# Optimization experiments

Measured on AMD Instinct MI355X. Metric: run time of the kernel, lower is better.

Reference implementation:

```python
import jax, jax.numpy as jnp
import numpy as np

B, S, D, H, E = 1, 2048, 1024, 16, 65536
HD = D // H
LN_EPS = 1e-5


def setup_inputs() -> dict:
    key = jax.random.key(0)
    ks = jax.random.split(key, 18)
    s = 0.02
    inp = {
        'x': jax.random.normal(ks[0], (B, S, D), jnp.float32),
        'node_types': jax.random.uniform(ks[1], (B, S, 2), jnp.float32),
        'stoichiometry': jax.random.normal(ks[2], (E,), jnp.float32),
        'Wq': s * jax.random.normal(ks[3], (D, D), jnp.float32),
        'bq': jnp.zeros((D,), jnp.float32),
        'Wk': s * jax.random.normal(ks[4], (D, D), jnp.float32),
        'bk': jnp.zeros((D,), jnp.float32),
        'Wv': s * jax.random.normal(ks[5], (D, D), jnp.float32),
        'bv': jnp.zeros((D,), jnp.float32),
        'Wo': s * jax.random.normal(ks[6], (D, D), jnp.float32),
        'bo': jnp.zeros((D,), jnp.float32),
        'Wn1': s * jax.random.normal(ks[7], (D // 2, D + 2), jnp.float32),
        'bn1': jnp.zeros((D // 2,), jnp.float32),
        'Wn2': s * jax.random.normal(ks[8], (H, D // 2), jnp.float32),
        'bn2': jnp.zeros((H,), jnp.float32),
        'ln_g': jnp.ones((D,), jnp.float32),
        'ln_b': jnp.zeros((D,), jnp.float32),
        'edge_index': jax.random.randint(ks[9], (2, E), 0, S, jnp.int64),
    }
    return inp


def _layer_norm(y, g, b):
    m = jnp.mean(y, axis=-1, keepdims=True)
    v = jnp.mean(jnp.square(y - m), axis=-1, keepdims=True)
    return (y - m) * jax.lax.rsqrt(v + LN_EPS) * g + b


def reference(x, node_types, stoichiometry, Wq, bq, Wk, bk, Wv, bv, Wo, bo,
              Wn1, bn1, Wn2, bn2, ln_g, ln_b, edge_index):
    b, s, d = x.shape
    h, hd = H, d // H
    # QKV projections -> [b, h, s, hd]
    Q = (x @ Wq.T + bq).reshape(b, s, h, hd).transpose(0, 2, 1, 3)
    K = (x @ Wk.T + bk).reshape(b, s, h, hd).transpose(0, 2, 1, 3)
    V = (x @ Wv.T + bv).reshape(b, s, h, hd).transpose(0, 2, 1, 3)
    scores = jnp.einsum('bhqd,bhkd->bhqk', Q, K) / np.sqrt(hd)  # [b,h,s,s]
    # node-type attention MLP -> per-node, per-head weights [b,s,h]
    nt_in = jnp.concatenate([x, node_types], axis=-1)
    ntw = jax.nn.softmax(jax.nn.relu(nt_in @ Wn1.T + bn1) @ Wn2.T + bn2, axis=-1)
    # applied as per-head, per-key multiplicative mask [b,h,1,s]
    scores = scores * ntw.transpose(0, 2, 1)[:, :, None, :]
    # dense stoichiometric mask via edge scatter [s,s]
    stoich_mask = jnp.zeros((s, s), x.dtype).at[edge_index[0], edge_index[1]].set(stoichiometry)
    scores = scores * stoich_mask[None, None]
    attn = jax.nn.softmax(scores, axis=-1)  # dropout = identity (eval)
    out = jnp.einsum('bhqk,bhkd->bhqd', attn, V).transpose(0, 2, 1, 3).reshape(b, s, d)
    out = out @ Wo.T + bo
    y = _layer_norm(x + out, ln_g, ln_b)
    return (y, attn)
```

## Files before the change

### kernel.cpp

```cpp
#include <hip/hip_runtime.h>
#include <hip/hip_bf16.h>

#define S 2048
#define D 1024
#define NH 16
#define HD 64
#define NE 65536
#define DH 512
#define SLOTS 128

typedef __attribute__((ext_vector_type(8))) short short8;
typedef __attribute__((ext_vector_type(4))) float f32x4;

#define MFMA16(a, b, c) __builtin_amdgcn_mfma_f32_16x16x32_bf16(a, b, c, 0, 0, 0)

__device__ __forceinline__ unsigned short f2bf(float f) {
    __hip_bfloat16 h = __float2bfloat16(f);
    return *reinterpret_cast<unsigned short*>(&h);
}
__device__ __forceinline__ float bf2f(unsigned short u) {
    unsigned int x = ((unsigned int)u) << 16;
    return *reinterpret_cast<float*>(&x);
}

__device__ __forceinline__ void gload16(const unsigned short* g, unsigned short* l) {
    __builtin_amdgcn_global_load_lds(
        (const __attribute__((address_space(1))) unsigned int*)g,
        (__attribute__((address_space(3))) unsigned int*)l, 16, 0, 0);
}

__global__ __launch_bounds__(256) void k_prep(const float* __restrict__ x,
                                              const float* __restrict__ Wq,
                                              const float* __restrict__ Wk,
                                              const float* __restrict__ Wv,
                                              const float* __restrict__ Wn1,
                                              const float* __restrict__ Wo,
                                              const float* __restrict__ bq,
                                              const float* __restrict__ bk,
                                              const float* __restrict__ bv,
                                              const float* __restrict__ bn1,
                                              unsigned short* __restrict__ xb,
                                              unsigned short* __restrict__ wb,
                                              float* __restrict__ biasAll,
                                              int* __restrict__ rowcnt) {
    int row = blockIdx.x, z = blockIdx.y, t = threadIdx.x;
    if (z == 5) {
        if (row < 14) {
            int g = row * 256 + t;
            float v = (g < 1024) ? bq[g]
                    : (g < 2048) ? bk[g - 1024]
                    : (g < 3072) ? bv[g - 2048] : bn1[g - 3072];
            biasAll[g] = v;
        } else if (row >= 16 && row < 24) {
            rowcnt[(row - 16) * 256 + t] = 0;
        }
        return;
    }
    if (z >= 6) {
        int s = (z - 6) * 1024 + row;
        const float* r = x + (long)s * 1024;
        unsigned short* o = xb + (long)s * 1024;
#pragma unroll
        for (int j = 0; j < 4; j++) o[t * 4 + j] = f2bf(r[t * 4 + j]);
        return;
    }
    if (z == 3 && row >= DH) return;
    const float* src;
    long stride = 1024;
    if (z == 0) src = Wq;
    else if (z == 1) src = Wk;
    else if (z == 2) src = Wv;
    else if (z == 3) { src = Wn1; stride = 1026; }
    else src = Wo;
    const float* r = src + (long)row * stride;
    unsigned short* o = wb + (long)z * 1048576 + (long)row * 1024;
#pragma unroll
    for (int j = 0; j < 4; j++) o[t * 4 + j] = f2bf(r[t * 4 + j]);
}

__global__ __launch_bounds__(256) void k_scatter_csr(const int* __restrict__ ei,
                                                     const float* __restrict__ st,
                                                     int* __restrict__ rowcnt,
                                                     int* __restrict__ cpack,
                                                     float* __restrict__ cval) {
    int e = blockIdx.x * 256 + threadIdx.x;
    int r = ei[e], c = ei[NE + e];
    int i = atomicAdd(&rowcnt[r], 1);
    if (i < SLOTS) {
        cpack[r * SLOTS + i] = ((e + 1) << 11) | c;
        cval[r * SLOTS + i] = st[e];
    }
}

__global__ __launch_bounds__(256) void k_gemm_fused(const unsigned short* __restrict__ A,
                                                    const unsigned short* __restrict__ Bw,
                                                    const float* __restrict__ biasAll,
                                                    unsigned short* __restrict__ qout,
                                                    unsigned short* __restrict__ kout,
                                                    unsigned short* __restrict__ vout,
                                                    float* __restrict__ hidden) {
    __shared__ unsigned short Als[128 * 64];
    __shared__ unsigned short Bls[128 * 64];
    const int tid = threadIdx.x, w = tid >> 6, lane = tid & 63;
    const int l15 = lane & 15, lhi = lane >> 4;
    const int wr = w >> 1, wc = w & 1;
    const int m0 = blockIdx.x * 128, n0 = blockIdx.y * 128;
    f32x4 acc[4][4] = {};
    for (int kt = 0; kt < 16; kt++) {
        __syncthreads();
#pragma unroll
        for (int i = 0; i < 4; i++) {
            int reg = i * 4 + w;
            int idx = reg * 64 + lane;
            int row = idx >> 3, c8 = (idx & 7) * 8;
            gload16(A + (long)(m0 + row) * 1024 + kt * 64 + c8, Als + reg * 512);
            gload16(Bw + (long)(n0 + row) * 1024 + kt * 64 + c8, Bls + reg * 512);
        }
        asm volatile("s_waitcnt vmcnt(0)");
        __syncthreads();
#pragma unroll
        for (int kk = 0; kk < 2; kk++) {
            short8 a[4], b[4];
#pragma unroll
            for (int mi = 0; mi < 4; mi++)
                a[mi] = *reinterpret_cast<const short8*>(Als + (wr * 64 + mi * 16 + l15) * 64 + kk * 32 + lhi * 8);
#pragma unroll
            for (int ni = 0; ni < 4; ni++)
                b[ni] = *reinterpret_cast<const short8*>(Bls + (wc * 64 + ni * 16 + l15) * 64 + kk * 32 + lhi * 8);
#pragma unroll
            for (int mi = 0; mi < 4; mi++)
#pragma unroll
                for (int ni = 0; ni < 4; ni++)
                    acc[mi][ni] = MFMA16(a[mi], b[ni], acc[mi][ni]);
        }
    }
#pragma unroll
    for (int ni = 0; ni < 4; ni++) {
        int n = n0 + wc * 64 + ni * 16 + l15;
        float bb = biasAll[n];
#pragma unroll
        for (int mi = 0; mi < 4; mi++) {
#pragma unroll
            for (int r = 0; r < 4; r++) {
                int m = m0 + wr * 64 + mi * 16 + lhi * 4 + r;
                float v = acc[mi][ni][r] + bb;
                if (n < 3072) {
                    int z = n >> 10, c = n & 1023;
                    int hh = c >> 6, hd = c & 63;
                    unsigned short* dst = (z == 0) ? qout : ((z == 1) ? kout : vout);
                    dst[(long)hh * S * HD + (long)m * HD + hd] = f2bf(v);
                } else {
                    hidden[(long)m * DH + (n - 3072)] = v;
                }
            }
        }
    }
}

__global__ __launch_bounds__(256) void k_gemm_out(const unsigned short* __restrict__ A,
                                                  const unsigned short* __restrict__ Bw,
                                                  const float* __restrict__ bo,
                                                  float* __restrict__ proj) {
    __shared__ unsigned short Als[128 * 64];
    __shared__ unsigned short Bls[64 * 64];
    const int tid = threadIdx.x, w = tid >> 6, lane = tid & 63;
    const int l15 = lane & 15, lhi = lane >> 4;
    const int wr = w >> 1, wc = w & 1;
    const int m0 = blockIdx.x * 128, n0 = blockIdx.y * 64;
    f32x4 acc[4][2] = {};
    for (int kt = 0; kt < 16; kt++) {
        __syncthreads();
#pragma unroll
        for (int i = 0; i < 4; i++) {
            int reg = i * 4 + w;
            int idx = reg * 64 + lane;
            int row = idx >> 3, c8 = (idx & 7) * 8;
            gload16(A + (long)(m0 + row) * 1024 + kt * 64 + c8, Als + reg * 512);
        }
#pragma unroll
        for (int i = 0; i < 2; i++) {
            int reg = i * 4 + w;
            int idx = reg * 64 + lane;
            int row = idx >> 3, c8 = (idx & 7) * 8;
            gload16(Bw + (long)(n0 + row) * 1024 + kt * 64 + c8, Bls + reg * 512);
        }
        asm volatile("s_waitcnt vmcnt(0)");
        __syncthreads();
#pragma unroll
        for (int kk = 0; kk < 2; kk++) {
            short8 a[4], b[2];
#pragma unroll
            for (int mi = 0; mi < 4; mi++)
                a[mi] = *reinterpret_cast<const short8*>(Als + (wr * 64 + mi * 16 + l15) * 64 + kk * 32 + lhi * 8);
#pragma unroll
            for (int ni = 0; ni < 2; ni++)
                b[ni] = *reinterpret_cast<const short8*>(Bls + (wc * 32 + ni * 16 + l15) * 64 + kk * 32 + lhi * 8);
#pragma unroll
            for (int mi = 0; mi < 4; mi++)
#pragma unroll
                for (int ni = 0; ni < 2; ni++)
                    acc[mi][ni] = MFMA16(a[mi], b[ni], acc[mi][ni]);
        }
    }
#pragma unroll
    for (int ni = 0; ni < 2; ni++) {
        int n = n0 + wc * 32 + ni * 16 + l15;
        float bb = bo[n];
#pragma unroll
        for (int mi = 0; mi < 4; mi++) {
#pragma unroll
            for (int r = 0; r < 4; r++) {
                int m = m0 + wr * 64 + mi * 16 + lhi * 4 + r;
                proj[(long)m * 1024 + n] = acc[mi][ni][r] + bb;
            }
        }
    }
}

__global__ __launch_bounds__(256) void k_ntw(const float* __restrict__ hidden,
                                             const float* __restrict__ Wn1,
                                             const float* __restrict__ nt,
                                             const float* __restrict__ Wn2,
                                             const float* __restrict__ bn2,
                                             const unsigned short* __restrict__ vb,
                                             float* __restrict__ ntwT,
                                             float* __restrict__ vsump) {
    int tid = threadIdx.x;
    if (blockIdx.x >= 2048) {
        int idx = blockIdx.x - 2048;
        int h = idx >> 3, j = idx & 7;
        int w = tid >> 6, lane = tid & 63;
        __shared__ float p[4][64];
        float acc = 0.f;
        int r0 = j * 256 + w * 64;
        for (int k = 0; k < 64; k++)
            acc += bf2f(vb[((long)h * S + r0 + k) * HD + lane]);
        p[w][lane] = acc;
        __syncthreads();
        if (tid < 64) vsump[(h * 8 + j) * 64 + tid] = p[0][tid] + p[1][tid] + p[2][tid] + p[3][tid];
        return;
    }
    int s = blockIdx.x;
    __shared__ float rh[DH];
    __shared__ float part[16][17];
    float nt0 = nt[s * 2 + 0], nt1 = nt[s * 2 + 1];
    for (int j = tid; j < DH; j += 256) {
        float v = hidden[(long)s * DH + j] + nt0 * Wn1[(long)j * 1026 + 1024]
                + nt1 * Wn1[(long)j * 1026 + 1025];
        rh[j] = fmaxf(v, 0.f);
    }
    __syncthreads();
    {
        int hh = tid & 15, ch = tid >> 4;
        float p2 = 0.f;
#pragma unroll
        for (int j = 0; j < 32; j++) p2 += rh[ch * 32 + j] * Wn2[hh * DH + ch * 32 + j];
        part[ch][hh] = p2;
    }
    __syncthreads();
    if (tid < 16) {
        float l = bn2[tid];
#pragma unroll
        for (int c = 0; c < 16; c++) l += part[c][tid];
        float mx = l;
#pragma unroll
        for (int m = 1; m < 16; m <<= 1) mx = fmaxf(mx, __shfl_xor(mx, m));
        float e = __expf(l - mx);
        float sum = e;
#pragma unroll
        for (int m = 1; m < 16; m <<= 1) sum += __shfl_xor(sum, m);
        ntwT[tid * S + s] = e / sum;
    }
}

__global__ __launch_bounds__(256, 4) void k_sparsefill(const unsigned short* __restrict__ qb,
                                                       const unsigned short* __restrict__ kb,
                                                       const unsigned short* __restrict__ vb,
                                                       const float* __restrict__ ntwT,
                                                       const int* __restrict__ rowcnt,
                                                       const int* __restrict__ cpack,
                                                       const float* __restrict__ cval,
                                                       const float* __restrict__ vsump,
                                                       float* __restrict__ attn_out,
                                                       unsigned short* __restrict__ pv_out) {
    __shared__ int c_lds[4][SLOTS];
    __shared__ float pd_lds[4][SLOTS];
    __shared__ unsigned char alive_lds[4][SLOTS];
    const int tid = threadIdx.x, w = tid >> 6, lane = tid & 63;
    int b = (int)blockIdx.x;
    b = (b & 7) * 1024 + (b >> 3);
    const int r = b * 4 + w;
    const int h = r >> 11, q = r & 2047;
    const int i_loc = lane & 15, dpart = lane >> 4;
    const int nnz_raw = rowcnt[q];
    const int nnz = nnz_raw < SLOTS ? nnz_raw : SLOTS;
    const int chunks = (nnz + 15) >> 4;

    for (int i = lane; i < nnz; i += 64) c_lds[w][i] = cpack[q * SLOTS + i];
    asm volatile("" ::: "memory");

    int myCnt = 0;
    for (int i = lane; i < nnz; i += 64) {
        int pk = c_lds[w][i];
        bool alive = true;
        for (int j = 0; j < nnz; j++) {
            int pj = c_lds[w][j];
            if ((((pj ^ pk) & 2047) == 0) && pj > pk) alive = false;
        }
        alive_lds[w][i] = alive ? 1 : 0;
        myCnt += alive ? 1 : 0;
    }
#pragma unroll
    for (int off = 1; off < 64; off <<= 1) myCnt += __shfl_xor(myCnt, off);
    const int nnz_alive = myCnt;
    asm volatile("" ::: "memory");

    float qf[16];
    {
        const unsigned short* qp = qb + ((long)h * S + q) * HD + dpart * 16;
        short8 q0 = *reinterpret_cast<const short8*>(qp);
        short8 q1 = *reinterpret_cast<const short8*>(qp + 8);
#pragma unroll
        for (int j = 0; j < 8; j++) {
            qf[j] = bf2f((unsigned short)q0[j]);
            qf[8 + j] = bf2f((unsigned short)q1[j]);
        }
    }

    float s_reg[8], e_reg[8];
    int c_reg[8];
    int vmask = 0;
#pragma unroll
    for (int c8 = 0; c8 < 8; c8++) {
        s_reg[c8] = -3.0e38f;
        c_reg[c8] = 0;
        if (c8 < chunks) {
            int i = c8 * 16 + i_loc;
            bool inr = i < nnz;
            int ig = inr ? i : 0;
            bool valid = inr && alive_lds[w][ig];
            int c = c_lds[w][ig] & 2047;
            float vv = cval[q * SLOTS + ig];
            const unsigned short* kp = kb + ((long)h * S + c) * HD + dpart * 16;
            short8 k0 = *reinterpret_cast<const short8*>(kp);
            short8 k1 = *reinterpret_cast<const short8*>(kp + 8);
            float dot = 0.f;
#pragma unroll
            for (int j = 0; j < 8; j++) {
                dot += qf[j] * bf2f((unsigned short)k0[j]);
                dot += qf[8 + j] * bf2f((unsigned short)k1[j]);
            }
            dot += __shfl_xor(dot, 16);
            dot += __shfl_xor(dot, 32);
            if (valid) {
                s_reg[c8] = dot * 0.125f * ntwT[(long)h * S + c] * vv;
                c_reg[c8] = c;
                vmask |= 1 << c8;
            }
        }
    }

    float m = s_reg[0];
#pragma unroll
    for (int c8 = 1; c8 < 8; c8++) m = fmaxf(m, s_reg[c8]);
    m = fmaxf(m, __shfl_xor(m, 1));
    m = fmaxf(m, __shfl_xor(m, 2));
    m = fmaxf(m, __shfl_xor(m, 4));
    m = fmaxf(m, __shfl_xor(m, 8));
    const float gm = fmaxf(m, 0.f);

    float zs = 0.f;
#pragma unroll
    for (int c8 = 0; c8 < 8; c8++) {
        e_reg[c8] = __expf(s_reg[c8] - gm);
        zs += e_reg[c8];
    }
    zs += __shfl_xor(zs, 1);
    zs += __shfl_xor(zs, 2);
    zs += __shfl_xor(zs, 4);
    zs += __shfl_xor(zs, 8);
    const float e0 = __expf(-gm);
    const float Z = zs + (float)(S - nnz_alive) * e0;
    const float inv = 1.0f / Z;
    const float p0 = e0 * inv;

    if (dpart == 0) {
#pragma unroll
        for (int c8 = 0; c8 < 8; c8++) {
            int i = c8 * 16 + i_loc;
            if (c8 < chunks && i < nnz)
                pd_lds[w][i] = ((vmask >> c8) & 1) ? e_reg[c8] * inv - p0 : 0.f;
        }
    }
    asm volatile("" ::: "memory");

    float* arow = attn_out + (long)r * S;
    float4* a4 = reinterpret_cast<float4*>(arow) + lane;
    const float4 f4 = {p0, p0, p0, p0};
#pragma unroll
    for (int u = 0; u < 8; u++) a4[u * 64] = f4;
    __threadfence_block();
    if (dpart == 0) {
#pragma unroll
        for (int c8 = 0; c8 < 8; c8++)
            if ((vmask >> c8) & 1) arow[c_reg[c8]] = e_reg[c8] * inv;
    }

    float vacc = 0.f;
    for (int i = 0; i < nnz; i++) {
        int c = c_lds[w][i] & 2047;
        float pd = pd_lds[w][i];
        vacc += pd * bf2f(vb[((long)h * S + c) * HD + lane]);
    }
    float vs = 0.f;
#pragma unroll
    for (int j = 0; j < 8; j++) vs += vsump[(h * 8 + j) * 64 + lane];
    vacc += p0 * vs;
    pv_out[(long)q * D + h * HD + lane] = f2bf(vacc);
}

__global__ __launch_bounds__(256) void k_ln(const float* __restrict__ x,
                                            const float* __restrict__ proj,
                                            const float* __restrict__ g,
                                            const float* __restrict__ bta,
                                            float* __restrict__ y) {
    int s = blockIdx.x, tid = threadIdx.x;
    int w = tid >> 6, lane = tid & 63;
    __shared__ float red[8];
    float4 xv = reinterpret_cast<const float4*>(x + (long)s * 1024)[tid];
    float4 pv = reinterpret_cast<const float4*>(proj + (long)s * 1024)[tid];
    float t0 = xv.x + pv.x, t1 = xv.y + pv.y, t2 = xv.z + pv.z, t3 = xv.w + pv.w;
    float lsum = t0 + t1 + t2 + t3;
#pragma unroll
    for (int m = 32; m >= 1; m >>= 1) lsum += __shfl_xor(lsum, m);
    if (lane == 0) red[w] = lsum;
    __syncthreads();
    float mean = (red[0] + red[1] + red[2] + red[3]) * (1.0f / 1024.f);
    float d0 = t0 - mean, d1 = t1 - mean, d2 = t2 - mean, d3 = t3 - mean;
    float lvar = d0 * d0 + d1 * d1 + d2 * d2 + d3 * d3;
#pragma unroll
    for (int m = 32; m >= 1; m >>= 1) lvar += __shfl_xor(lvar, m);
    if (lane == 0) red[4 + w] = lvar;
    __syncthreads();
    float var = (red[4] + red[5] + red[6] + red[7]) * (1.0f / 1024.f);
    float rstd = rsqrtf(var + 1e-5f);
    float4 gv = reinterpret_cast<const float4*>(g)[tid];
    float4 bv = reinterpret_cast<const float4*>(bta)[tid];
    float4 out;
    out.x = d0 * rstd * gv.x + bv.x;
    out.y = d1 * rstd * gv.y + bv.y;
    out.z = d2 * rstd * gv.z + bv.z;
    out.w = d3 * rstd * gv.w + bv.w;
    reinterpret_cast<float4*>(y + (long)s * 1024)[tid] = out;
}

extern "C" void kernel_launch(void* const* d_in, const int* in_sizes, int n_in,
                              void* d_out, int out_size, void* d_ws, size_t ws_size,
                              hipStream_t stream) {
    const float* x = (const float*)d_in[0];
    const float* node_types = (const float*)d_in[1];
    const float* stoich = (const float*)d_in[2];
    const float* Wq = (const float*)d_in[3];
    const float* bq = (const float*)d_in[4];
    const float* Wk = (const float*)d_in[5];
    const float* bk = (const float*)d_in[6];
    const float* Wv = (const float*)d_in[7];
    const float* bv = (const float*)d_in[8];
    const float* Wo = (const float*)d_in[9];
    const float* bo = (const float*)d_in[10];
    const float* Wn1 = (const float*)d_in[11];
    const float* bn1 = (const float*)d_in[12];
    const float* Wn2 = (const float*)d_in[13];
    const float* bn2 = (const float*)d_in[14];
    const float* ln_g = (const float*)d_in[15];
    const float* ln_b = (const float*)d_in[16];
    const int* ei = (const int*)d_in[17];

    char* ws = (char*)d_ws;
    unsigned short* x_bf = (unsigned short*)(ws);
    unsigned short* q_bf = (unsigned short*)(ws + (4l << 20));
    unsigned short* k_bf = (unsigned short*)(ws + (8l << 20));
    unsigned short* v_bf = (unsigned short*)(ws + (12l << 20));
    unsigned short* w_bf = (unsigned short*)(ws + (16l << 20));
    float* hidden = (float*)(ws + (26l << 20));
    float* ntwT = (float*)(ws + (30l << 20));
    int* rowcnt = (int*)(ws + (30l << 20) + (192l << 10));
    float* vsump = (float*)(ws + (30l << 20) + (384l << 10));
    float* biasAll = (float*)(ws + (30l << 20) + (448l << 10));
    int* cpack = (int*)(ws + (31l << 20));
    float* cval = (float*)(ws + (32l << 20));
    unsigned short* pvb = (unsigned short*)(ws + (49l << 20));
    float* proj = (float*)(ws + (53l << 20));

    float* y_out = (float*)d_out;
    float* attn_out = (float*)d_out + (long)S * D;

    k_prep<<<dim3(1024, 8), 256, 0, stream>>>(x, Wq, Wk, Wv, Wn1, Wo,
                                              bq, bk, bv, bn1, x_bf, w_bf,
                                              biasAll, rowcnt);
    k_scatter_csr<<<256, 256, 0, stream>>>(ei, stoich, rowcnt, cpack, cval);
    k_gemm_fused<<<dim3(16, 28), 256, 0, stream>>>(x_bf, w_bf, biasAll,
                                                   q_bf, k_bf, v_bf, hidden);
    k_ntw<<<2176, 256, 0, stream>>>(hidden, Wn1, node_types, Wn2, bn2, v_bf,
                                    ntwT, vsump);
    k_sparsefill<<<8192, 256, 0, stream>>>(q_bf, k_bf, v_bf, ntwT, rowcnt,
                                           cpack, cval, vsump, attn_out, pvb);
    k_gemm_out<<<dim3(16, 16), 256, 0, stream>>>(pvb, w_bf + 4l * 1048576, bo, proj);
    k_ln<<<2048, 256, 0, stream>>>(x, proj, ln_g, ln_b, y_out);
}
```

Before: 161.3 us.

## Fuse edge scatter and V column sums into the QKV GEMM kernel

```diff
diff --git a/kernel.cpp b/kernel.cpp
--- a/kernel.cpp
+++ b/kernel.cpp
@@ -42,7 +42,8 @@
                                               unsigned short* __restrict__ xb,
                                               unsigned short* __restrict__ wb,
                                               float* __restrict__ biasAll,
-                                              int* __restrict__ rowcnt) {
+                                              int* __restrict__ rowcnt,
+                                              float* __restrict__ vsumf) {
     int row = blockIdx.x, z = blockIdx.y, t = threadIdx.x;
     if (z == 5) {
         if (row < 14) {
@@ -53,6 +54,8 @@
             biasAll[g] = v;
         } else if (row >= 16 && row < 24) {
             rowcnt[(row - 16) * 256 + t] = 0;
+        } else if (row >= 24 && row < 28) {
+            vsumf[(row - 24) * 256 + t] = 0.f;
         }
         return;
     }
@@ -78,27 +81,33 @@
     for (int j = 0; j < 4; j++) o[t * 4 + j] = f2bf(r[t * 4 + j]);
 }
 
-__global__ __launch_bounds__(256) void k_scatter_csr(const int* __restrict__ ei,
-                                                     const float* __restrict__ st,
-                                                     int* __restrict__ rowcnt,
-                                                     int* __restrict__ cpack,
-                                                     float* __restrict__ cval) {
-    int e = blockIdx.x * 256 + threadIdx.x;
-    int r = ei[e], c = ei[NE + e];
-    int i = atomicAdd(&rowcnt[r], 1);
-    if (i < SLOTS) {
-        cpack[r * SLOTS + i] = ((e + 1) << 11) | c;
-        cval[r * SLOTS + i] = st[e];
-    }
-}
-
 __global__ __launch_bounds__(256) void k_gemm_fused(const unsigned short* __restrict__ A,
                                                     const unsigned short* __restrict__ Bw,
                                                     const float* __restrict__ biasAll,
+                                                    const int* __restrict__ ei,
+                                                    const float* __restrict__ st,
+                                                    int* __restrict__ rowcnt,
+                                                    int* __restrict__ cpack,
+                                                    float* __restrict__ cval,
+                                                    float* __restrict__ vsumf,
                                                     unsigned short* __restrict__ qout,
                                                     unsigned short* __restrict__ kout,
                                                     unsigned short* __restrict__ vout,
                                                     float* __restrict__ hidden) {
+    if (blockIdx.y == 28) {
+        int base = blockIdx.x * 4096 + threadIdx.x;
+#pragma unroll
+        for (int k = 0; k < 16; k++) {
+            int e = base + k * 256;
+            int r = ei[e], c = ei[NE + e];
+            int i = atomicAdd(&rowcnt[r], 1);
+            if (i < SLOTS) {
+                cpack[r * SLOTS + i] = ((e + 1) << 11) | c;
+                cval[r * SLOTS + i] = st[e];
+            }
+        }
+        return;
+    }
     __shared__ unsigned short Als[128 * 64];
     __shared__ unsigned short Bls[128 * 64];
     const int tid = threadIdx.x, w = tid >> 6, lane = tid & 63;
@@ -138,12 +147,14 @@
     for (int ni = 0; ni < 4; ni++) {
         int n = n0 + wc * 64 + ni * 16 + l15;
         float bb = biasAll[n];
+        float colsum = 0.f;
 #pragma unroll
         for (int mi = 0; mi < 4; mi++) {
 #pragma unroll
             for (int r = 0; r < 4; r++) {
                 int m = m0 + wr * 64 + mi * 16 + lhi * 4 + r;
                 float v = acc[mi][ni][r] + bb;
+                colsum += v;
                 if (n < 3072) {
                     int z = n >> 10, c = n & 1023;
                     int hh = c >> 6, hd = c & 63;
@@ -153,6 +164,11 @@
                     hidden[(long)m * DH + (n - 3072)] = v;
                 }
             }
+        }
+        if (n >= 2048 && n < 3072) {
+            colsum += __shfl_xor(colsum, 16);
+            colsum += __shfl_xor(colsum, 32);
+            if (lhi == 0) atomicAdd(&vsumf[n - 2048], colsum);
         }
     }
 }
@@ -222,24 +238,8 @@
                                              const float* __restrict__ nt,
                                              const float* __restrict__ Wn2,
                                              const float* __restrict__ bn2,
-                                             const unsigned short* __restrict__ vb,
-                                             float* __restrict__ ntwT,
-                                             float* __restrict__ vsump) {
+                                             float* __restrict__ ntwT) {
     int tid = threadIdx.x;
-    if (blockIdx.x >= 2048) {
-        int idx = blockIdx.x - 2048;
-        int h = idx >> 3, j = idx & 7;
-        int w = tid >> 6, lane = tid & 63;
-        __shared__ float p[4][64];
-        float acc = 0.f;
-        int r0 = j * 256 + w * 64;
-        for (int k = 0; k < 64; k++)
-            acc += bf2f(vb[((long)h * S + r0 + k) * HD + lane]);
-        p[w][lane] = acc;
-        __syncthreads();
-        if (tid < 64) vsump[(h * 8 + j) * 64 + tid] = p[0][tid] + p[1][tid] + p[2][tid] + p[3][tid];
-        return;
-    }
     int s = blockIdx.x;
     __shared__ float rh[DH];
     __shared__ float part[16][17];
@@ -280,7 +280,7 @@
                                                        const int* __restrict__ rowcnt,
                                                        const int* __restrict__ cpack,
                                                        const float* __restrict__ cval,
-                                                       const float* __restrict__ vsump,
+                                                       const float* __restrict__ vsumf,
                                                        float* __restrict__ attn_out,
                                                        unsigned short* __restrict__ pv_out) {
     __shared__ int c_lds[4][SLOTS];
@@ -395,10 +395,10 @@
     asm volatile("" ::: "memory");
 
     float* arow = attn_out + (long)r * S;
-    float4* a4 = reinterpret_cast<float4*>(arow) + lane;
-    const float4 f4 = {p0, p0, p0, p0};
-#pragma unroll
-    for (int u = 0; u < 8; u++) a4[u * 64] = f4;
+    f32x4* a4 = reinterpret_cast<f32x4*>(arow) + lane;
+    const f32x4 f4 = {p0, p0, p0, p0};
+#pragma unroll
+    for (int u = 0; u < 8; u++) __builtin_nontemporal_store(f4, a4 + u * 64);
     __threadfence_block();
     if (dpart == 0) {
 #pragma unroll
@@ -412,10 +412,7 @@
         float pd = pd_lds[w][i];
         vacc += pd * bf2f(vb[((long)h * S + c) * HD + lane]);
     }
-    float vs = 0.f;
-#pragma unroll
-    for (int j = 0; j < 8; j++) vs += vsump[(h * 8 + j) * 64 + lane];
-    vacc += p0 * vs;
+    vacc += p0 * vsumf[h * HD + lane];
     pv_out[(long)q * D + h * HD + lane] = f2bf(vacc);
 }
 
@@ -485,7 +482,7 @@
     float* hidden = (float*)(ws + (26l << 20));
     float* ntwT = (float*)(ws + (30l << 20));
     int* rowcnt = (int*)(ws + (30l << 20) + (192l << 10));
-    float* vsump = (float*)(ws + (30l << 20) + (384l << 10));
+    float* vsumf = (float*)(ws + (30l << 20) + (384l << 10));
     float* biasAll = (float*)(ws + (30l << 20) + (448l << 10));
     int* cpack = (int*)(ws + (31l << 20));
     float* cval = (float*)(ws + (32l << 20));
@@ -497,14 +494,13 @@
 
     k_prep<<<dim3(1024, 8), 256, 0, stream>>>(x, Wq, Wk, Wv, Wn1, Wo,
                                               bq, bk, bv, bn1, x_bf, w_bf,
-                                              biasAll, rowcnt);
-    k_scatter_csr<<<256, 256, 0, stream>>>(ei, stoich, rowcnt, cpack, cval);
-    k_gemm_fused<<<dim3(16, 28), 256, 0, stream>>>(x_bf, w_bf, biasAll,
-                                                   q_bf, k_bf, v_bf, hidden);
-    k_ntw<<<2176, 256, 0, stream>>>(hidden, Wn1, node_types, Wn2, bn2, v_bf,
-                                    ntwT, vsump);
+                                              biasAll, rowcnt, vsumf);
+    k_gemm_fused<<<dim3(16, 29), 256, 0, stream>>>(x_bf, w_bf, biasAll,
+                                                   ei, stoich, rowcnt, cpack, cval,
+                                                   vsumf, q_bf, k_bf, v_bf, hidden);
+    k_ntw<<<2048, 256, 0, stream>>>(hidden, Wn1, node_types, Wn2, bn2, ntwT);
     k_sparsefill<<<8192, 256, 0, stream>>>(q_bf, k_bf, v_bf, ntwT, rowcnt,
-                                           cpack, cval, vsump, attn_out, pvb);
+                                           cpack, cval, vsumf, attn_out, pvb);
     k_gemm_out<<<dim3(16, 16), 256, 0, stream>>>(pvb, w_bf + 4l * 1048576, bo, proj);
     k_ln<<<2048, 256, 0, stream>>>(x, proj, ln_g, ln_b, y_out);
 }
```

Measured after the change: 154.9 us. 3.9% less time.
